# Performance work log

Hardware: AMD Instinct MI355X
Metric: run time of the kernel (lower is better)

Reference implementation:

```python
import jax, jax.numpy as jnp
import numpy as np

D_MODEL = 1024
NUM_HEADS = 16
DEPTH = D_MODEL // NUM_HEADS
NEG_INF_SCALE = -1e9


def setup_inputs() -> dict:
    key = jax.random.key(0)
    ks = jax.random.split(key, 12)
    B, S = 2, 2048
    q = jax.random.normal(ks[0], (B, S, D_MODEL), dtype=jnp.float32)
    k = jax.random.normal(ks[1], (B, S, D_MODEL), dtype=jnp.float32)
    v = jax.random.normal(ks[2], (B, S, D_MODEL), dtype=jnp.float32)
    # causal mask: 1 where attention is disallowed (future positions)
    mask = jnp.triu(jnp.ones((S, S), dtype=jnp.float32), k=1)[None, None]
    scale = 1.0 / np.sqrt(D_MODEL)
    Wq = jax.random.normal(ks[3], (D_MODEL, D_MODEL), dtype=jnp.float32) * scale
    bq = jnp.zeros((D_MODEL,), dtype=jnp.float32)
    Wk = jax.random.normal(ks[4], (D_MODEL, D_MODEL), dtype=jnp.float32) * scale
    bk = jnp.zeros((D_MODEL,), dtype=jnp.float32)
    Wv = jax.random.normal(ks[5], (D_MODEL, D_MODEL), dtype=jnp.float32) * scale
    bv = jnp.zeros((D_MODEL,), dtype=jnp.float32)
    Wo = jax.random.normal(ks[6], (D_MODEL, D_MODEL), dtype=jnp.float32) * scale
    bo = jnp.zeros((D_MODEL,), dtype=jnp.float32)
    return {"v": v, "k": k, "q": q, "mask": mask,
            "Wq": Wq, "bq": bq, "Wk": Wk, "bk": bk,
            "Wv": Wv, "bv": bv, "Wo": Wo, "bo": bo}


def _split_heads(x):
    B, S, _ = x.shape
    return x.reshape(B, S, NUM_HEADS, DEPTH).transpose(0, 2, 1, 3)  # [B,H,S,depth]


def reference(v, k, q, mask, Wq, bq, Wk, bk, Wv, bv, Wo, bo):
    B, Sq, _ = q.shape
    qh = _split_heads(q @ Wq + bq)  # [B,H,Sq,depth]
    kh = _split_heads(k @ Wk + bk)  # [B,H,Sk,depth]
    vh = _split_heads(v @ Wv + bv)  # [B,H,Sk,depth]
    logits = jnp.einsum('bhqd,bhkd->bhqk', qh, kh) / jnp.sqrt(
        jnp.asarray(DEPTH, dtype=jnp.float32))
    logits = logits + mask * NEG_INF_SCALE
    attn = jax.nn.softmax(logits, axis=-1)
    out = jnp.einsum('bhqk,bhkd->bhqd', attn, vh)  # [B,H,Sq,depth]
    out = out.transpose(0, 2, 1, 3).reshape(B, Sq, D_MODEL)
    return out @ Wo + bo
```

## Files before the change

kernel.cpp:

```cpp
#include <hip/hip_runtime.h>
#include <stdint.h>

#define D_MODEL 1024
#define NHEADS  16
#define DEPTH   64
#define BATCH   2
#define SEQ     2048
#define M_TOT   (BATCH * SEQ)

#define Q_SCALE 0.18033688011112042f

typedef unsigned short u16;
typedef unsigned int   u32;
typedef __attribute__((ext_vector_type(8))) short bf16x8;
typedef __attribute__((ext_vector_type(4))) float f32x4;

__device__ __forceinline__ float bf2f(unsigned int u) {
    union { unsigned int i; float f; } x;
    x.i = (u & 0xffffu) << 16;
    return x.f;
}
__device__ __forceinline__ u16 f2bf(float f) {
    union { float f; unsigned int i; } x;
    x.f = f;
    unsigned int lsb = (x.i >> 16) & 1u;
    x.i += 0x7fffu + lsb;
    return (u16)(x.i >> 16);
}
__device__ __forceinline__ u32 fbits(float f) {
    union { float f; unsigned int i; } x; x.f = f; return x.i;
}
__device__ __forceinline__ float exp2f_hw(float x) {
    return __builtin_amdgcn_exp2f(x);
}

template <int CTRL>
__device__ __forceinline__ float dppf(float x) {
    int r = __builtin_amdgcn_update_dpp(0, (int)fbits(x), CTRL, 0xF, 0xF, false);
    union { int i; float f; } u; u.i = r; return u.f;
}
__device__ __forceinline__ float redmax16(float x) {
    x = fmaxf(x, dppf<0xB1>(x));
    x = fmaxf(x, dppf<0x4E>(x));
    x = fmaxf(x, dppf<0x124>(x));
    x = fmaxf(x, dppf<0x128>(x));
    return x;
}
__device__ __forceinline__ float redsum16(float x) {
    x += dppf<0xB1>(x);
    x += dppf<0x4E>(x);
    x += dppf<0x124>(x);
    x += dppf<0x128>(x);
    return x;
}

__device__ __forceinline__ void stage16(const u16* g, u16* ldsbase) {
#if __has_builtin(__builtin_amdgcn_global_load_lds)
    __builtin_amdgcn_global_load_lds(
        (const __attribute__((address_space(1))) unsigned int*)g,
        (__attribute__((address_space(3))) unsigned int*)ldsbase, 16, 0, 0);
#else
    int lane = threadIdx.x & 63;
    *(uint4*)(ldsbase + lane * 8) = *(const uint4*)g;
#endif
}

__global__ void sniff_kernel(const u16* __restrict__ q, int* __restrict__ flag) {
    const int t = threadIdx.x;
    int cnt = 0;
    #pragma unroll
    for (int j = 0; j < 4; ++j) {
        unsigned int bits = q[2 * (t + 64 * j)];
        bool susp = ((bits & 0x7fffu) >= 0x4780u);
        cnt += (int)__popcll(__ballot(susp));
    }
    if (t == 0) flag[0] = (cnt >= 32) ? 1 : 0;
}

__global__ __launch_bounds__(256)
void conv_kernel(const void* s0, const void* s1, const void* s2,
                 u16* d0, u16* d1, u16* d2, const int* __restrict__ flag) {
    const int z = blockIdx.z;
    const void* src = (z == 0) ? s0 : (z == 1) ? s1 : s2;
    u16* dst = (z == 0) ? d0 : (z == 1) ? d1 : d2;
    const int f32 = *flag;
    const size_t i = ((size_t)blockIdx.x * 256 + threadIdx.x) * 8;
    if (f32) {
        const float* s = (const float*)src + i;
        float4 a = *(const float4*)s;
        float4 b = *(const float4*)(s + 4);
        u16 t8[8];
        t8[0] = f2bf(a.x); t8[1] = f2bf(a.y); t8[2] = f2bf(a.z); t8[3] = f2bf(a.w);
        t8[4] = f2bf(b.x); t8[5] = f2bf(b.y); t8[6] = f2bf(b.z); t8[7] = f2bf(b.w);
        *(uint4*)(dst + i) = *(uint4*)t8;
    } else {
        *(uint4*)(dst + i) = *(const uint4*)((const u16*)src + i);
    }
}

__global__ __launch_bounds__(256)
void wT_kernel(const void* W0, const void* W1, const void* W2, const void* W3,
               u16* T0, u16* T1, u16* T2, u16* T3, const int* __restrict__ flag) {
    __shared__ u16 t[64][72];
    const int z = blockIdx.z;
    const void* Wv = (z == 0) ? W0 : (z == 1) ? W1 : (z == 2) ? W2 : W3;
    u16* WT = (z == 0) ? T0 : (z == 1) ? T1 : (z == 2) ? T2 : T3;
    const int f32 = *flag;
    const int tid = threadIdx.x;
    const int n0 = blockIdx.x * 64, k0 = blockIdx.y * 64;

    #pragma unroll
    for (int cb = 0; cb < 2; ++cb) {
        int c = tid + cb * 256;
        int kl = c >> 3, nc = (c & 7) * 8;
        size_t off = (size_t)(k0 + kl) * D_MODEL + n0 + nc;
        u16 tmp[8];
        if (f32) {
            const float* W = (const float*)Wv;
            float4 a = *(const float4*)(W + off);
            float4 b = *(const float4*)(W + off + 4);
            tmp[0] = f2bf(a.x); tmp[1] = f2bf(a.y); tmp[2] = f2bf(a.z); tmp[3] = f2bf(a.w);
            tmp[4] = f2bf(b.x); tmp[5] = f2bf(b.y); tmp[6] = f2bf(b.z); tmp[7] = f2bf(b.w);
        } else {
            *(uint4*)tmp = *(const uint4*)((const u16*)Wv + off);
        }
        *(uint4*)&t[kl][nc] = *(uint4*)tmp;
    }
    __syncthreads();
    #pragma unroll
    for (int cb = 0; cb < 2; ++cb) {
        int c = tid + cb * 256;
        int nl = c >> 3, kc = (c & 7) * 8;
        u16 tmp[8];
        #pragma unroll
        for (int i = 0; i < 8; ++i) tmp[i] = t[kc + i][nl];
        *(uint4*)(WT + (size_t)(n0 + nl) * D_MODEL + k0 + kc) = *(uint4*)tmp;
    }
}

struct GemmJob {
    const u16*  A;
    const u16*  BT;
    const void* bias;
    void*       C;
    int cmode;
    float scale;
};

__global__ __launch_bounds__(256)
void gemm6(GemmJob j0, GemmJob j1, GemmJob j2, const int* __restrict__ flag) {
    __shared__ u16 Als[128 * 64];
    __shared__ u16 Bls[128 * 64];

    const u32 lin = blockIdx.x + gridDim.x * (blockIdx.y + gridDim.y * blockIdx.z);
    const u32 xcd = lin & 7, idx = lin >> 3;
    const u32 per = (gridDim.y * gridDim.z) >> 3;
    const u32 mz = xcd * per + (idx >> 3);
    const u32 nb_ = idx & 7;
    const u32 zz = mz / gridDim.y;
    const u32 my = mz % gridDim.y;
    GemmJob jb = (zz == 0) ? j0 : (zz == 1) ? j1 : j2;

    const int f32 = *flag;
    const int tid = threadIdx.x;
    const int w = tid >> 6, lane = tid & 63;
    const int cc = lane & 15, quad = lane >> 4;
    const int wm = w >> 1, wn = w & 1;
    const int m0 = my * 128, n0 = nb_ * 128;

    f32x4 zero4 = {0.f, 0.f, 0.f, 0.f};
    f32x4 acc[4][4];
    #pragma unroll
    for (int i = 0; i < 4; ++i)
        #pragma unroll
        for (int j = 0; j < 4; ++j) acc[i][j] = zero4;

    const int srow_off = lane >> 3;
    const int sg8 = ((lane & 7) ^ ((lane >> 3) & 7)) * 8;

    for (int k0 = 0; k0 < D_MODEL; k0 += 64) {
        __syncthreads();
        #pragma unroll
        for (int i = 0; i < 4; ++i) {
            int c = w * 4 + i;
            int row = c * 8 + srow_off;
            stage16(jb.BT + (size_t)(n0 + row) * D_MODEL + k0 + sg8, &Bls[c * 512]);
            stage16(jb.A  + (size_t)(m0 + row) * D_MODEL + k0 + sg8, &Als[c * 512]);
        }
        __syncthreads();

        const int sw = cc & 7;
        bf16x8 af[4][2], bf[4][2];
        #pragma unroll
        for (int i = 0; i < 4; ++i) {
            const u16* ar = &Als[(wm * 64 + i * 16 + cc) * 64];
            af[i][0] = *(const bf16x8*)(ar + ((quad ^ sw) * 8));
            af[i][1] = *(const bf16x8*)(ar + (((4 + quad) ^ sw) * 8));
        }
        #pragma unroll
        for (int j = 0; j < 4; ++j) {
            const u16* br = &Bls[(wn * 64 + j * 16 + cc) * 64];
            bf[j][0] = *(const bf16x8*)(br + ((quad ^ sw) * 8));
            bf[j][1] = *(const bf16x8*)(br + (((4 + quad) ^ sw) * 8));
        }
        #pragma unroll
        for (int i = 0; i < 4; ++i)
            #pragma unroll
            for (int j = 0; j < 4; ++j) {
                acc[i][j] = __builtin_amdgcn_mfma_f32_16x16x32_bf16(af[i][0], bf[j][0], acc[i][j], 0, 0, 0);
                acc[i][j] = __builtin_amdgcn_mfma_f32_16x16x32_bf16(af[i][1], bf[j][1], acc[i][j], 0, 0, 0);
            }
    }

    #pragma unroll
    for (int j = 0; j < 4; ++j) {
        int col = n0 + wn * 64 + j * 16 + cc;
        float bv = f32 ? ((const float*)jb.bias)[col] : bf2f(((const u16*)jb.bias)[col]);
        #pragma unroll
        for (int i = 0; i < 4; ++i)
            #pragma unroll
            for (int r = 0; r < 4; ++r) {
                int row = m0 + wm * 64 + i * 16 + quad * 4 + r;
                float vo = (acc[i][j][r] + bv) * jb.scale;
                if (jb.cmode == 0) {
                    ((u16*)jb.C)[(size_t)row * D_MODEL + col] = f2bf(vo);
                } else if (jb.cmode == 1) {
                    int bb = row >> 11, tok = row & (SEQ - 1);
                    int hh = col >> 6, dd = col & 63;
                    int tile = tok >> 6, n = tok & 63;
                    int kap = ((n & 15) << 2) + (n >> 4);
                    ((u16*)jb.C)[((size_t)((bb * NHEADS + hh) * DEPTH + dd)) * SEQ
                                 + tile * 64 + kap] = f2bf(vo);
                } else {
                    if (f32) ((float*)jb.C)[(size_t)row * D_MODEL + col] = vo;
                    else     ((u16*)jb.C)[(size_t)row * D_MODEL + col] = f2bf(vo);
                }
            }
    }
}

__global__ __launch_bounds__(256, 3)
void attn3(const u16* __restrict__ Qp, const u16* __restrict__ Kp,
           const u16* __restrict__ VpT, u16* __restrict__ Ao) {
    __shared__ u16 Kls[2][64 * 64];
    __shared__ u16 Vls[2][64 * 64];
    __shared__ u16 Pls[4][32][72];

    const int tid = threadIdx.x;
    const int w = tid >> 6, lane = tid & 63;
    const int cc = lane & 15, quad = lane >> 4;
    const int qt = (int)(gridDim.x - 1 - blockIdx.x);
    const int h = blockIdx.y, b = blockIdx.z;
    const int qbase = qt * 128 + w * 32;

    bf16x8 qf[2][2];
    #pragma unroll
    for (int mi = 0; mi < 2; ++mi) {
        const u16* qr = Qp + (size_t)(b * SEQ + qbase + mi * 16 + cc) * D_MODEL + h * DEPTH;
        qf[mi][0] = *(const bf16x8*)(qr + quad * 8);
        qf[mi][1] = *(const bf16x8*)(qr + 32 + quad * 8);
    }

    const u16* kbase = Kp + (size_t)(b * SEQ) * D_MODEL + h * DEPTH;
    const u16* vbase = VpT + (size_t)((b * NHEADS + h) * DEPTH) * SEQ;

    const int r8 = lane >> 3;
    const int g8 = ((lane & 7) ^ (r8 & 7)) * 8;

    auto stageKV = [&](int buf, int jt) {
        #pragma unroll
        for (int i = 0; i < 2; ++i) {
            int row = w * 16 + i * 8 + r8;
            stage16(kbase + (size_t)(jt * 64 + row) * D_MODEL + g8,
                    &Kls[buf][(w * 16 + i * 8) * 64]);
            stage16(vbase + (size_t)row * SEQ + jt * 64 + g8,
                    &Vls[buf][(w * 16 + i * 8) * 64]);
        }
    };

    f32x4 zero4 = {0.f, 0.f, 0.f, 0.f};
    f32x4 oacc[2][4];
    #pragma unroll
    for (int mi = 0; mi < 2; ++mi)
        #pragma unroll
        for (int db = 0; db < 4; ++db) oacc[mi][db] = zero4;
    float m_run[2][4], l_run[2][4];
    #pragma unroll
    for (int mi = 0; mi < 2; ++mi)
        #pragma unroll
        for (int r = 0; r < 4; ++r) { m_run[mi][r] = -1e30f; l_run[mi][r] = 0.f; }

    const int jtmax = 2 * qt + 1;
    stageKV(0, 0);

    for (int jt = 0; jt <= jtmax; ++jt) {
        const int cur = jt & 1;
        __syncthreads();
        if (jt < jtmax) stageKV(cur ^ 1, jt + 1);

        if (jt * 64 > qbase + 31) continue;

        const int sw = cc & 7;
        bf16x8 kf[4][2];
        #pragma unroll
        for (int nb = 0; nb < 4; ++nb) {
            const u16* kr = &Kls[cur][(nb * 16 + cc) * 64];
            kf[nb][0] = *(const bf16x8*)(kr + ((quad ^ sw) * 8));
            kf[nb][1] = *(const bf16x8*)(kr + (((4 + quad) ^ sw) * 8));
        }
        f32x4 s[2][4];
        #pragma unroll
        for (int mi = 0; mi < 2; ++mi)
            #pragma unroll
            for (int nb = 0; nb < 4; ++nb) {
                s[mi][nb] = __builtin_amdgcn_mfma_f32_16x16x32_bf16(qf[mi][0], kf[nb][0], zero4, 0, 0, 0);
                s[mi][nb] = __builtin_amdgcn_mfma_f32_16x16x32_bf16(qf[mi][1], kf[nb][1], s[mi][nb], 0, 0, 0);
            }
        #pragma unroll
        for (int mi = 0; mi < 2; ++mi) {
            if (jt * 64 + 63 > qbase + mi * 16) {
                #pragma unroll
                for (int nb = 0; nb < 4; ++nb)
                    #pragma unroll
                    for (int r = 0; r < 4; ++r)
                        if (jt * 64 + nb * 16 + cc > qbase + mi * 16 + quad * 4 + r)
                            s[mi][nb][r] = -1e30f;
            }
        }

        float alpha[2][4];
        #pragma unroll
        for (int mi = 0; mi < 2; ++mi) {
            #pragma unroll
            for (int r = 0; r < 4; ++r) {
                float mrow = redmax16(fmaxf(fmaxf(s[mi][0][r], s[mi][1][r]),
                                            fmaxf(s[mi][2][r], s[mi][3][r])));
                float mn = fmaxf(m_run[mi][r], mrow);
                alpha[mi][r] = exp2f_hw(m_run[mi][r] - mn);
                m_run[mi][r] = mn;
            }
            #pragma unroll
            for (int nb = 0; nb < 4; ++nb)
                #pragma unroll
                for (int r = 0; r < 4; ++r)
                    s[mi][nb][r] = exp2f_hw(s[mi][nb][r] - m_run[mi][r]);
            #pragma unroll
            for (int r = 0; r < 4; ++r)
                l_run[mi][r] = l_run[mi][r] * alpha[mi][r]
                             + ((s[mi][0][r] + s[mi][1][r]) + (s[mi][2][r] + s[mi][3][r]));
            #pragma unroll
            for (int db = 0; db < 4; ++db)
                #pragma unroll
                for (int r = 0; r < 4; ++r)
                    oacc[mi][db][r] *= alpha[mi][r];
        }

        #pragma unroll
        for (int mi = 0; mi < 2; ++mi)
            #pragma unroll
            for (int r = 0; r < 4; ++r) {
                u32 p01 = __builtin_amdgcn_perm(fbits(s[mi][1][r]), fbits(s[mi][0][r]), 0x07060302u);
                u32 p23 = __builtin_amdgcn_perm(fbits(s[mi][3][r]), fbits(s[mi][2][r]), 0x07060302u);
                uint2 pk; pk.x = p01; pk.y = p23;
                *(uint2*)&Pls[w][mi * 16 + quad * 4 + r][4 * cc] = pk;
            }
        __asm__ volatile("" ::: "memory");

        bf16x8 pf[2][2];
        #pragma unroll
        for (int mi = 0; mi < 2; ++mi) {
            pf[mi][0] = *(const bf16x8*)&Pls[w][mi * 16 + cc][quad * 8];
            pf[mi][1] = *(const bf16x8*)&Pls[w][mi * 16 + cc][32 + quad * 8];
        }
        #pragma unroll
        for (int db = 0; db < 4; ++db) {
            const u16* vr = &Vls[cur][(db * 16 + cc) * 64];
            bf16x8 v0 = *(const bf16x8*)(vr + ((quad ^ sw) * 8));
            bf16x8 v1 = *(const bf16x8*)(vr + (((4 + quad) ^ sw) * 8));
            #pragma unroll
            for (int mi = 0; mi < 2; ++mi) {
                oacc[mi][db] = __builtin_amdgcn_mfma_f32_16x16x32_bf16(pf[mi][0], v0, oacc[mi][db], 0, 0, 0);
                oacc[mi][db] = __builtin_amdgcn_mfma_f32_16x16x32_bf16(pf[mi][1], v1, oacc[mi][db], 0, 0, 0);
            }
        }
    }

    #pragma unroll
    for (int mi = 0; mi < 2; ++mi) {
        float linv[4];
        #pragma unroll
        for (int r = 0; r < 4; ++r) linv[r] = 1.0f / redsum16(l_run[mi][r]);
        #pragma unroll
        for (int db = 0; db < 4; ++db)
            #pragma unroll
            for (int r = 0; r < 4; ++r) {
                size_t row = (size_t)(b * SEQ + qbase + mi * 16 + quad * 4 + r);
                Ao[row * D_MODEL + h * DEPTH + db * 16 + cc] =
                    f2bf(oacc[mi][db][r] * linv[r]);
            }
    }
}

extern "C" void kernel_launch(void* const* d_in, const int* in_sizes, int n_in,
                              void* d_out, int out_size, void* d_ws, size_t ws_size,
                              hipStream_t stream) {
    const void* v  = d_in[0];
    const void* k  = d_in[1];
    const void* q  = d_in[2];
    const void* Wq = d_in[4];
    const void* bq = d_in[5];
    const void* Wk = d_in[6];
    const void* bk = d_in[7];
    const void* Wv = d_in[8];
    const void* bv = d_in[9];
    const void* Wo = d_in[10];
    const void* bo = d_in[11];

    char* base = (char*)d_ws;
    int* flag = (int*)base;
    const size_t WSZ = (size_t)D_MODEL * D_MODEL;
    const size_t TOK = (size_t)M_TOT * D_MODEL;
    u16* WqT = (u16*)(base + 256);
    u16* WkT = WqT + WSZ;
    u16* WvT = WkT + WSZ;
    u16* WoT = WvT + WSZ;
    u16* Qb  = WoT + WSZ;
    u16* Kb  = Qb + TOK;
    u16* Vb  = Kb + TOK;
    u16* Qp  = Vb + TOK;
    u16* Kp  = Qp + TOK;
    u16* VpT = Kp + TOK;
    u16* Ao  = Qb;

    sniff_kernel<<<1, 64, 0, stream>>>((const u16*)q, flag);

    conv_kernel<<<dim3(2048, 1, 3), 256, 0, stream>>>(q, k, v, Qb, Kb, Vb, flag);
    wT_kernel<<<dim3(16, 16, 4), 256, 0, stream>>>(Wq, Wk, Wv, Wo,
                                                   WqT, WkT, WvT, WoT, flag);

    GemmJob jq = {Qb, WqT, bq, Qp,    0, Q_SCALE};
    GemmJob jk = {Kb, WkT, bk, Kp,    0, 1.0f};
    GemmJob jv = {Vb, WvT, bv, VpT,   1, 1.0f};
    gemm6<<<dim3(8, 32, 3), 256, 0, stream>>>(jq, jk, jv, flag);

    attn3<<<dim3(16, 16, 2), 256, 0, stream>>>(Qp, Kp, VpT, Ao);

    GemmJob jo = {Ao, WoT, bo, d_out, 2, 1.0f};
    gemm6<<<dim3(8, 32, 1), 256, 0, stream>>>(jo, jo, jo, flag);
}
```

Before: 301.2 us.

## Halve attention query tile to 64 rows and remap blocks longest-first

The attention kernel now gives each block 64 query rows (16 per wave) instead of 128, doubling the grid to 1024 blocks. Block indices are linearised so that the heaviest causal tiles (largest qq) are scheduled first across heads and batches. The causal mask is applied only on the diagonal tile, and the per-iteration skip branch is dropped. It also adds s_setprio around the MFMA sections. The aim is better load balance and occupancy in exchange for loading K/V tiles twice as often per query row.

```diff
diff --git a/kernel.cpp b/kernel.cpp
--- a/kernel.cpp
+++ b/kernel.cpp
@@ -244,21 +244,23 @@
            const u16* __restrict__ VpT, u16* __restrict__ Ao) {
     __shared__ u16 Kls[2][64 * 64];
     __shared__ u16 Vls[2][64 * 64];
-    __shared__ u16 Pls[4][32][72];
+    __shared__ u16 Pls[4][16][72];
 
     const int tid = threadIdx.x;
     const int w = tid >> 6, lane = tid & 63;
     const int cc = lane & 15, quad = lane >> 4;
-    const int qt = (int)(gridDim.x - 1 - blockIdx.x);
-    const int h = blockIdx.y, b = blockIdx.z;
-    const int qbase = qt * 128 + w * 32;
-
-    bf16x8 qf[2][2];
-    #pragma unroll
-    for (int mi = 0; mi < 2; ++mi) {
-        const u16* qr = Qp + (size_t)(b * SEQ + qbase + mi * 16 + cc) * D_MODEL + h * DEPTH;
-        qf[mi][0] = *(const bf16x8*)(qr + quad * 8);
-        qf[mi][1] = *(const bf16x8*)(qr + 32 + quad * 8);
+
+    const u32 lin = blockIdx.x + 32u * (blockIdx.y + 16u * blockIdx.z);
+    const int qq = 31 - (int)(lin >> 5);
+    const int h  = (int)(lin & 15);
+    const int b  = (int)((lin >> 4) & 1);
+    const int qbase = qq * 64 + w * 16;
+
+    bf16x8 qf[2];
+    {
+        const u16* qr = Qp + (size_t)(b * SEQ + qbase + cc) * D_MODEL + h * DEPTH;
+        qf[0] = *(const bf16x8*)(qr + quad * 8);
+        qf[1] = *(const bf16x8*)(qr + 32 + quad * 8);
     }
 
     const u16* kbase = Kp + (size_t)(b * SEQ) * D_MODEL + h * DEPTH;
@@ -279,26 +281,19 @@
     };
 
     f32x4 zero4 = {0.f, 0.f, 0.f, 0.f};
-    f32x4 oacc[2][4];
-    #pragma unroll
-    for (int mi = 0; mi < 2; ++mi)
-        #pragma unroll
-        for (int db = 0; db < 4; ++db) oacc[mi][db] = zero4;
-    float m_run[2][4], l_run[2][4];
-    #pragma unroll
-    for (int mi = 0; mi < 2; ++mi)
-        #pragma unroll
-        for (int r = 0; r < 4; ++r) { m_run[mi][r] = -1e30f; l_run[mi][r] = 0.f; }
-
-    const int jtmax = 2 * qt + 1;
+    f32x4 oacc[4];
+    #pragma unroll
+    for (int db = 0; db < 4; ++db) oacc[db] = zero4;
+    float m_run[4], l_run[4];
+    #pragma unroll
+    for (int r = 0; r < 4; ++r) { m_run[r] = -1e30f; l_run[r] = 0.f; }
+
     stageKV(0, 0);
 
-    for (int jt = 0; jt <= jtmax; ++jt) {
+    for (int jt = 0; jt <= qq; ++jt) {
         const int cur = jt & 1;
         __syncthreads();
-        if (jt < jtmax) stageKV(cur ^ 1, jt + 1);
-
-        if (jt * 64 > qbase + 31) continue;
+        if (jt < qq) stageKV(cur ^ 1, jt + 1);
 
         const int sw = cc & 7;
         bf16x8 kf[4][2];
@@ -308,97 +303,82 @@
             kf[nb][0] = *(const bf16x8*)(kr + ((quad ^ sw) * 8));
             kf[nb][1] = *(const bf16x8*)(kr + (((4 + quad) ^ sw) * 8));
         }
-        f32x4 s[2][4];
-        #pragma unroll
-        for (int mi = 0; mi < 2; ++mi)
-            #pragma unroll
-            for (int nb = 0; nb < 4; ++nb) {
-                s[mi][nb] = __builtin_amdgcn_mfma_f32_16x16x32_bf16(qf[mi][0], kf[nb][0], zero4, 0, 0, 0);
-                s[mi][nb] = __builtin_amdgcn_mfma_f32_16x16x32_bf16(qf[mi][1], kf[nb][1], s[mi][nb], 0, 0, 0);
-            }
-        #pragma unroll
-        for (int mi = 0; mi < 2; ++mi) {
-            if (jt * 64 + 63 > qbase + mi * 16) {
-                #pragma unroll
-                for (int nb = 0; nb < 4; ++nb)
-                    #pragma unroll
-                    for (int r = 0; r < 4; ++r)
-                        if (jt * 64 + nb * 16 + cc > qbase + mi * 16 + quad * 4 + r)
-                            s[mi][nb][r] = -1e30f;
-            }
-        }
-
-        float alpha[2][4];
-        #pragma unroll
-        for (int mi = 0; mi < 2; ++mi) {
-            #pragma unroll
-            for (int r = 0; r < 4; ++r) {
-                float mrow = redmax16(fmaxf(fmaxf(s[mi][0][r], s[mi][1][r]),
-                                            fmaxf(s[mi][2][r], s[mi][3][r])));
-                float mn = fmaxf(m_run[mi][r], mrow);
-                alpha[mi][r] = exp2f_hw(m_run[mi][r] - mn);
-                m_run[mi][r] = mn;
-            }
+        f32x4 s[4];
+        __builtin_amdgcn_s_setprio(1);
+        #pragma unroll
+        for (int nb = 0; nb < 4; ++nb) {
+            s[nb] = __builtin_amdgcn_mfma_f32_16x16x32_bf16(qf[0], kf[nb][0], zero4, 0, 0, 0);
+            s[nb] = __builtin_amdgcn_mfma_f32_16x16x32_bf16(qf[1], kf[nb][1], s[nb], 0, 0, 0);
+        }
+        __builtin_amdgcn_s_setprio(0);
+
+        if (jt == qq) {
             #pragma unroll
             for (int nb = 0; nb < 4; ++nb)
                 #pragma unroll
                 for (int r = 0; r < 4; ++r)
-                    s[mi][nb][r] = exp2f_hw(s[mi][nb][r] - m_run[mi][r]);
+                    if (nb * 16 + cc > w * 16 + quad * 4 + r) s[nb][r] = -1e30f;
+        }
+
+        float alpha[4];
+        #pragma unroll
+        for (int r = 0; r < 4; ++r) {
+            float mrow = redmax16(fmaxf(fmaxf(s[0][r], s[1][r]),
+                                        fmaxf(s[2][r], s[3][r])));
+            float mn = fmaxf(m_run[r], mrow);
+            alpha[r] = exp2f_hw(m_run[r] - mn);
+            m_run[r] = mn;
+        }
+        #pragma unroll
+        for (int nb = 0; nb < 4; ++nb)
             #pragma unroll
             for (int r = 0; r < 4; ++r)
-                l_run[mi][r] = l_run[mi][r] * alpha[mi][r]
-                             + ((s[mi][0][r] + s[mi][1][r]) + (s[mi][2][r] + s[mi][3][r]));
+                s[nb][r] = exp2f_hw(s[nb][r] - m_run[r]);
+        #pragma unroll
+        for (int r = 0; r < 4; ++r)
+            l_run[r] = l_run[r] * alpha[r]
+                     + ((s[0][r] + s[1][r]) + (s[2][r] + s[3][r]));
+        #pragma unroll
+        for (int db = 0; db < 4; ++db)
             #pragma unroll
-            for (int db = 0; db < 4; ++db)
-                #pragma unroll
-                for (int r = 0; r < 4; ++r)
-                    oacc[mi][db][r] *= alpha[mi][r];
-        }
-
-        #pragma unroll
-        for (int mi = 0; mi < 2; ++mi)
-            #pragma unroll
-            for (int r = 0; r < 4; ++r) {
-                u32 p01 = __builtin_amdgcn_perm(fbits(s[mi][1][r]), fbits(s[mi][0][r]), 0x07060302u);
-                u32 p23 = __builtin_amdgcn_perm(fbits(s[mi][3][r]), fbits(s[mi][2][r]), 0x07060302u);
-                uint2 pk; pk.x = p01; pk.y = p23;
-                *(uint2*)&Pls[w][mi * 16 + quad * 4 + r][4 * cc] = pk;
-            }
+            for (int r = 0; r < 4; ++r)
+                oacc[db][r] *= alpha[r];
+
+        #pragma unroll
+        for (int r = 0; r < 4; ++r) {
+            u32 p01 = __builtin_amdgcn_perm(fbits(s[1][r]), fbits(s[0][r]), 0x07060302u);
+            u32 p23 = __builtin_amdgcn_perm(fbits(s[3][r]), fbits(s[2][r]), 0x07060302u);
+            uint2 pk; pk.x = p01; pk.y = p23;
+            *(uint2*)&Pls[w][quad * 4 + r][4 * cc] = pk;
+        }
         __asm__ volatile("" ::: "memory");
 
-        bf16x8 pf[2][2];
-        #pragma unroll
-        for (int mi = 0; mi < 2; ++mi) {
-            pf[mi][0] = *(const bf16x8*)&Pls[w][mi * 16 + cc][quad * 8];
-            pf[mi][1] = *(const bf16x8*)&Pls[w][mi * 16 + cc][32 + quad * 8];
-        }
+        bf16x8 pf0 = *(const bf16x8*)&Pls[w][cc][quad * 8];
+        bf16x8 pf1 = *(const bf16x8*)&Pls[w][cc][32 + quad * 8];
+
+        __builtin_amdgcn_s_setprio(1);
         #pragma unroll
         for (int db = 0; db < 4; ++db) {
             const u16* vr = &Vls[cur][(db * 16 + cc) * 64];
             bf16x8 v0 = *(const bf16x8*)(vr + ((quad ^ sw) * 8));
             bf16x8 v1 = *(const bf16x8*)(vr + (((4 + quad) ^ sw) * 8));
-            #pragma unroll
-            for (int mi = 0; mi < 2; ++mi) {
-                oacc[mi][db] = __builtin_amdgcn_mfma_f32_16x16x32_bf16(pf[mi][0], v0, oacc[mi][db], 0, 0, 0);
-                oacc[mi][db] = __builtin_amdgcn_mfma_f32_16x16x32_bf16(pf[mi][1], v1, oacc[mi][db], 0, 0, 0);
-            }
-        }
-    }
-
-    #pragma unroll
-    for (int mi = 0; mi < 2; ++mi) {
-        float linv[4];
-        #pragma unroll
-        for (int r = 0; r < 4; ++r) linv[r] = 1.0f / redsum16(l_run[mi][r]);
-        #pragma unroll
-        for (int db = 0; db < 4; ++db)
-            #pragma unroll
-            for (int r = 0; r < 4; ++r) {
-                size_t row = (size_t)(b * SEQ + qbase + mi * 16 + quad * 4 + r);
-                Ao[row * D_MODEL + h * DEPTH + db * 16 + cc] =
-                    f2bf(oacc[mi][db][r] * linv[r]);
-            }
-    }
+            oacc[db] = __builtin_amdgcn_mfma_f32_16x16x32_bf16(pf0, v0, oacc[db], 0, 0, 0);
+            oacc[db] = __builtin_amdgcn_mfma_f32_16x16x32_bf16(pf1, v1, oacc[db], 0, 0, 0);
+        }
+        __builtin_amdgcn_s_setprio(0);
+    }
+
+    float linv[4];
+    #pragma unroll
+    for (int r = 0; r < 4; ++r) linv[r] = 1.0f / redsum16(l_run[r]);
+    #pragma unroll
+    for (int db = 0; db < 4; ++db)
+        #pragma unroll
+        for (int r = 0; r < 4; ++r) {
+            size_t row = (size_t)(b * SEQ + qbase + quad * 4 + r);
+            Ao[row * D_MODEL + h * DEPTH + db * 16 + cc] =
+                f2bf(oacc[db][r] * linv[r]);
+        }
 }
 
 extern "C" void kernel_launch(void* const* d_in, const int* in_sizes, int n_in,
@@ -443,7 +423,7 @@
     GemmJob jv = {Vb, WvT, bv, VpT,   1, 1.0f};
     gemm6<<<dim3(8, 32, 3), 256, 0, stream>>>(jq, jk, jv, flag);
 
-    attn3<<<dim3(16, 16, 2), 256, 0, stream>>>(Qp, Kp, VpT, Ao);
+    attn3<<<dim3(32, 16, 2), 256, 0, stream>>>(Qp, Kp, VpT, Ao);
 
     GemmJob jo = {Ao, WoT, bo, d_out, 2, 1.0f};
     gemm6<<<dim3(8, 32, 1), 256, 0, stream>>>(jo, jo, jo, flag);
```

After: 265.9 us. 11.7% less time.
